# Kernel optimization log

Hardware: AMD Instinct MI355X
Metric: run time of the kernel (lower is better)

The kernel has to match this reference:

```python
import jax, jax.numpy as jnp
import numpy as np


def setup_inputs() -> dict:
    key = jax.random.key(0)
    ks = jax.random.split(key, 6)
    B, T, C, H, E = 4, 2048, 768, 3072, 16
    scale = 0.02
    return {
        "x": jax.random.normal(ks[0], (B, T, C), dtype=jnp.float32),
        "w_shared_fc": jax.random.normal(ks[1], (C, 2 * H), dtype=jnp.float32) * scale,
        "w_shared_proj": jax.random.normal(ks[2], (H, C), dtype=jnp.float32) * scale,
        "w_experts_fc": jax.random.normal(ks[3], (E, C, 2 * H), dtype=jnp.float32) * scale,
        "w_experts_proj": jax.random.normal(ks[4], (E, H, C), dtype=jnp.float32) * scale,
        "w_gate": jax.random.normal(ks[5], (C, E), dtype=jnp.float32) * scale,
        "expert_bias": jnp.zeros((E,), dtype=jnp.float32),
        "top_k": 4,
    }


def _swiglu(h):
    gate, val = jnp.split(h, 2, axis=-1)
    return jax.nn.silu(gate) * val


def reference(x, w_shared_fc, w_shared_proj, w_experts_fc, w_experts_proj,
              w_gate, expert_bias, top_k):
    B, T, C = x.shape
    E = expert_bias.shape[0]
    N = B * T

    # shared expert (applied to every token)
    shared = _swiglu(x @ w_shared_fc) @ w_shared_proj  # [B,T,C]

    # top-k sigmoid routing
    gate_logits = x @ w_gate + expert_bias            # [B,T,E]
    gate_w = jax.nn.sigmoid(gate_logits)
    top_w, top_idx = jax.lax.top_k(gate_w, top_k)     # [B,T,K]
    top_w = top_w / jnp.sum(top_w, axis=-1, keepdims=True)

    # dense per-token/per-expert weight matrix [N,E] (zero for unrouted)
    w_dense = jnp.sum(jax.nn.one_hot(top_idx, E, dtype=x.dtype) * top_w[..., None],
                      axis=-2).reshape(N, E)

    flat_x = x.reshape(N, C)

    def body(acc, params):
        wfc, wproj, we = params  # [C,2H], [H,C], [N]
        out = _swiglu(flat_x @ wfc) @ wproj  # [N,C]
        return acc + we[:, None] * out, None

    routed, _ = jax.lax.scan(body, jnp.zeros_like(flat_x),
                             (w_experts_fc, w_experts_proj, w_dense.T))
    return shared + routed.reshape(B, T, C)
```

## Files before the change

kernel.cpp:

```cpp
#include <hip/hip_runtime.h>
#include <hip/hip_bf16.h>

typedef __hip_bfloat16 bf16;
typedef __attribute__((ext_vector_type(8))) short short8;
typedef __attribute__((ext_vector_type(4))) float float4v;

#define BM 128
#define BK 32

__device__ __forceinline__ void gload16(const bf16* g, bf16* s) {
    __builtin_amdgcn_global_load_lds(
        (const __attribute__((address_space(1))) void*)g,
        (__attribute__((address_space(3))) void*)s, 16, 0, 0);
}


__global__ void k_zero_cnt(int* cnt) {
    if (threadIdx.x < 16) cnt[threadIdx.x] = 0;
}

__global__ void k_convert_x(const float* __restrict__ in, bf16* __restrict__ out, int n) {
    int i = (blockIdx.x * blockDim.x + threadIdx.x) * 4;
    if (i + 3 < n) {
        float4 v = *(const float4*)(in + i);
        out[i + 0] = __float2bfloat16(v.x);
        out[i + 1] = __float2bfloat16(v.y);
        out[i + 2] = __float2bfloat16(v.z);
        out[i + 3] = __float2bfloat16(v.w);
    }
}

__global__ void k_transpose(const float* __restrict__ in, bf16* __restrict__ out,
                            int R, int S) {
    __shared__ float tile[32][33];
    size_t mat = (size_t)blockIdx.z * R * S;
    int s0 = blockIdx.x * 32, r0 = blockIdx.y * 32;
    int tx = threadIdx.x, ty = threadIdx.y;
    #pragma unroll
    for (int i = 0; i < 32; i += 8)
        tile[ty + i][tx] = in[mat + (size_t)(r0 + ty + i) * S + s0 + tx];
    __syncthreads();
    #pragma unroll
    for (int i = 0; i < 32; i += 8)
        out[mat + (size_t)(s0 + ty + i) * R + r0 + tx] = __float2bfloat16(tile[tx][ty + i]);
}

__global__ void k_gate(const float* __restrict__ x, const float* __restrict__ wg,
                       const float* __restrict__ bias, int* __restrict__ cnt,
                       int* __restrict__ tok, float* __restrict__ wl) {
    __shared__ float gates[16][17];
    int t = threadIdx.x;
    int tl = t >> 4;
    int e = t & 15;
    int token = blockIdx.x * 16 + tl;
    const float* xr = x + (size_t)token * 768;
    float acc = 0.f;
    #pragma unroll 4
    for (int c = 0; c < 768; ++c) acc += xr[c] * wg[c * 16 + e];
    acc += bias[e];
    gates[tl][e] = 1.f / (1.f + expf(-acc));
    __syncthreads();
    if (t < 16) {
        int token2 = blockIdx.x * 16 + t;
        float g[16];
        #pragma unroll
        for (int j = 0; j < 16; ++j) g[j] = gates[t][j];
        int idx[4]; float w[4]; float sum = 0.f;
        #pragma unroll
        for (int k = 0; k < 4; ++k) {
            float best = -1e30f; int bi = 0;
            #pragma unroll
            for (int j = 0; j < 16; ++j)
                if (g[j] > best) { best = g[j]; bi = j; }
            idx[k] = bi; w[k] = best; sum += best; g[bi] = -1e30f;
        }
        float inv = 1.f / sum;
        for (int k = 0; k < 4; ++k) {
            int slot = atomicAdd(&cnt[idx[k]], 1);
            tok[(idx[k] << 13) + slot] = token2;
            wl[(idx[k] << 13) + slot] = w[k] * inv;
        }
    }
}

__global__ void k_offsets(const int* __restrict__ cnt, int* __restrict__ offs) {
    if (threadIdx.x == 0) {
        int s = 0;
        for (int e = 0; e < 16; ++e) { offs[e] = s; s += cnt[e]; }
    }
}

template<int GATHER>
__global__ __launch_bounds__(256) void k_fc_swiglu(
    const bf16* __restrict__ A, const bf16* __restrict__ BT,
    bf16* __restrict__ act, const int* __restrict__ cnt,
    const int* __restrict__ offs, const int* __restrict__ tok) {
    const int Kd = 768, H = 3072;
    int e = blockIdx.z;
    int m0 = blockIdx.y * BM;
    int n0 = blockIdx.x * 64;
    int M;
    size_t actbase = 0;
    const int* tl = nullptr;
    if (GATHER) {
        M = cnt[e];
        if (m0 >= M) return;
        tl = tok + (e << 13);
        actbase = (size_t)offs[e] * H;
        BT += (size_t)e * 6144 * Kd;
    } else {
        M = 8192;
    }

    __shared__ bf16 sA[BM * BK];
    __shared__ bf16 sBg[64 * BK];
    __shared__ bf16 sBv[64 * BK];

    int tid = threadIdx.x;
    int lane = tid & 63;
    int w = tid >> 6;
    int wm = w & 1, wn = w >> 1;

    int cA0 = (w << 6) + lane;
    int cA1 = 256 + cA0;
    int cB = (w << 6) + lane;

    int rA0 = cA0 >> 2, rA1 = cA1 >> 2, rB = cB >> 2;
    int kA0 = (cA0 & 3) * 8, kA1 = (cA1 & 3) * 8, kB = (cB & 3) * 8;

    int grA0, grA1;
    if (GATHER) {
        grA0 = tl[min(m0 + rA0, M - 1)];
        grA1 = tl[min(m0 + rA1, M - 1)];
    } else {
        grA0 = m0 + rA0; grA1 = m0 + rA1;
    }

    const bf16* gA0 = A + (size_t)grA0 * Kd + kA0;
    const bf16* gA1 = A + (size_t)grA1 * Kd + kA1;
    const bf16* gBg = BT + (size_t)(n0 + rB) * Kd + kB;
    const bf16* gBv = BT + (size_t)(H + n0 + rB) * Kd + kB;
    bf16* sA0p = sA + cA0 * 8;
    bf16* sA1p = sA + cA1 * 8;
    bf16* sBgp = sBg + cB * 8;
    bf16* sBvp = sBv + cB * 8;

    float4v ag[4][2] = {};
    float4v av[4][2] = {};
    int quad = lane >> 4, l16 = lane & 15;

    for (int k0 = 0; k0 < Kd; k0 += BK) {
        __syncthreads();
        gload16(gA0 + k0, sA0p);
        gload16(gA1 + k0, sA1p);
        gload16(gBg + k0, sBgp);
        gload16(gBv + k0, sBvp);
        __syncthreads();
        short8 af[4], bg[2], bv[2];
        #pragma unroll
        for (int mf = 0; mf < 4; ++mf)
            af[mf] = *(const short8*)(sA + ((wm * 64 + mf * 16 + l16) * BK + quad * 8));
        #pragma unroll
        for (int nf = 0; nf < 2; ++nf) {
            bg[nf] = *(const short8*)(sBg + ((wn * 32 + nf * 16 + l16) * BK + quad * 8));
            bv[nf] = *(const short8*)(sBv + ((wn * 32 + nf * 16 + l16) * BK + quad * 8));
        }
        #pragma unroll
        for (int mf = 0; mf < 4; ++mf)
            #pragma unroll
            for (int nf = 0; nf < 2; ++nf) {
                ag[mf][nf] = __builtin_amdgcn_mfma_f32_16x16x32_bf16(af[mf], bg[nf], ag[mf][nf], 0, 0, 0);
                av[mf][nf] = __builtin_amdgcn_mfma_f32_16x16x32_bf16(af[mf], bv[nf], av[mf][nf], 0, 0, 0);
            }
    }

    #pragma unroll
    for (int mf = 0; mf < 4; ++mf)
        #pragma unroll
        for (int nf = 0; nf < 2; ++nf)
            #pragma unroll
            for (int r = 0; r < 4; ++r) {
                int mrow = m0 + wm * 64 + mf * 16 + quad * 4 + r;
                if (GATHER && mrow >= M) continue;
                int col = n0 + wn * 32 + nf * 16 + l16;
                float g = ag[mf][nf][r];
                float v = av[mf][nf][r];
                float sg = g / (1.f + __expf(-g));
                act[actbase + (size_t)mrow * H + col] = __float2bfloat16(sg * v);
            }
}

template<int ROUTED>
__global__ __launch_bounds__(256) void k_proj(
    const bf16* __restrict__ Aact, const bf16* __restrict__ PT,
    float* __restrict__ out, const int* __restrict__ cnt,
    const int* __restrict__ offs, const int* __restrict__ tok,
    const float* __restrict__ wl) {
    const int Kd = 3072;
    int e = blockIdx.z;
    int m0 = blockIdx.y * BM;
    int n0 = blockIdx.x * BM;
    int M;
    size_t abase = 0;
    if (ROUTED) {
        M = cnt[e];
        if (m0 >= M) return;
        abase = (size_t)offs[e] * Kd;
        PT += (size_t)e * 768 * Kd;
    } else {
        M = 8192;
    }

    __shared__ bf16 sA[BM * BK];
    __shared__ bf16 sB[BM * BK];

    int tid = threadIdx.x, lane = tid & 63, w = tid >> 6;
    int wm = w & 1, wn = w >> 1;
    int c0 = (w << 6) + lane;
    int c1 = 256 + c0;
    int r0 = c0 >> 2, r1 = c1 >> 2;
    int k0c = (c0 & 3) * 8, k1c = (c1 & 3) * 8;

    int ra0 = min(m0 + r0, M - 1);
    int ra1 = min(m0 + r1, M - 1);
    const bf16* gA0 = Aact + abase + (size_t)ra0 * Kd + k0c;
    const bf16* gA1 = Aact + abase + (size_t)ra1 * Kd + k1c;
    const bf16* gB0 = PT + (size_t)(n0 + r0) * Kd + k0c;
    const bf16* gB1 = PT + (size_t)(n0 + r1) * Kd + k1c;
    bf16* sA0p = sA + c0 * 8;
    bf16* sA1p = sA + c1 * 8;
    bf16* sB0p = sB + c0 * 8;
    bf16* sB1p = sB + c1 * 8;

    float4v acc[4][4] = {};
    int quad = lane >> 4, l16 = lane & 15;

    for (int kk = 0; kk < Kd; kk += BK) {
        __syncthreads();
        gload16(gA0 + kk, sA0p);
        gload16(gA1 + kk, sA1p);
        gload16(gB0 + kk, sB0p);
        gload16(gB1 + kk, sB1p);
        __syncthreads();
        short8 af[4], bb[4];
        #pragma unroll
        for (int i = 0; i < 4; ++i) {
            af[i] = *(const short8*)(sA + ((wm * 64 + i * 16 + l16) * BK + quad * 8));
            bb[i] = *(const short8*)(sB + ((wn * 64 + i * 16 + l16) * BK + quad * 8));
        }
        #pragma unroll
        for (int mf = 0; mf < 4; ++mf)
            #pragma unroll
            for (int nf = 0; nf < 4; ++nf)
                acc[mf][nf] = __builtin_amdgcn_mfma_f32_16x16x32_bf16(af[mf], bb[nf], acc[mf][nf], 0, 0, 0);
    }

    #pragma unroll
    for (int mf = 0; mf < 4; ++mf) {
        #pragma unroll
        for (int r = 0; r < 4; ++r) {
            int mr = m0 + wm * 64 + mf * 16 + quad * 4 + r;
            if (ROUTED) {
                if (mr < M) {
                    int t = tok[(e << 13) + mr];
                    float wgt = wl[(e << 13) + mr];
                    #pragma unroll
                    for (int nf = 0; nf < 4; ++nf) {
                        int col = n0 + wn * 64 + nf * 16 + l16;
                        atomicAdd(out + (size_t)t * 768 + col, wgt * acc[mf][nf][r]);
                    }
                }
            } else {
                #pragma unroll
                for (int nf = 0; nf < 4; ++nf) {
                    int col = n0 + wn * 64 + nf * 16 + l16;
                    out[(size_t)mr * 768 + col] = acc[mf][nf][r];
                }
            }
        }
    }
}


extern "C" void kernel_launch(void* const* d_in, const int* in_sizes, int n_in,
                              void* d_out, int out_size, void* d_ws, size_t ws_size,
                              hipStream_t stream) {
    const float* x    = (const float*)d_in[0];
    const float* wfc  = (const float*)d_in[1];
    const float* wpr  = (const float*)d_in[2];
    const float* wefc = (const float*)d_in[3];
    const float* wepr = (const float*)d_in[4];
    const float* wg   = (const float*)d_in[5];
    const float* eb   = (const float*)d_in[6];
    float* out = (float*)d_out;

    char* p = (char*)d_ws;
    bf16* x_bf  = (bf16*)p; p += (size_t)8192 * 768 * 2;
    bf16* fcT_s = (bf16*)p; p += (size_t)6144 * 768 * 2;
    bf16* prT_s = (bf16*)p; p += (size_t)768 * 3072 * 2;
    bf16* fcT_e = (bf16*)p; p += (size_t)16 * 6144 * 768 * 2;
    bf16* prT_e = (bf16*)p; p += (size_t)16 * 768 * 3072 * 2;
    bf16* act_s = (bf16*)p; p += (size_t)8192 * 3072 * 2;
    bf16* act_r = (bf16*)p; p += (size_t)32768 * 3072 * 2;
    int* cnt    = (int*)p;  p += 64;
    int* offs   = (int*)p;  p += 64;
    int* tok    = (int*)p;  p += (size_t)16 * 8192 * 4;
    float* wl   = (float*)p; p += (size_t)16 * 8192 * 4;

    k_zero_cnt<<<dim3(1), dim3(64), 0, stream>>>(cnt);
    k_convert_x<<<dim3(6144), dim3(256), 0, stream>>>(x, x_bf, 8192 * 768);
    k_transpose<<<dim3(192, 24, 1), dim3(32, 8), 0, stream>>>(wfc, fcT_s, 768, 6144);
    k_transpose<<<dim3(24, 96, 1), dim3(32, 8), 0, stream>>>(wpr, prT_s, 3072, 768);
    k_transpose<<<dim3(192, 24, 16), dim3(32, 8), 0, stream>>>(wefc, fcT_e, 768, 6144);
    k_transpose<<<dim3(24, 96, 16), dim3(32, 8), 0, stream>>>(wepr, prT_e, 3072, 768);
    k_gate<<<dim3(512), dim3(256), 0, stream>>>(x, wg, eb, cnt, tok, wl);
    k_offsets<<<dim3(1), dim3(64), 0, stream>>>(cnt, offs);

    k_fc_swiglu<0><<<dim3(48, 64, 1), dim3(256), 0, stream>>>(x_bf, fcT_s, act_s, cnt, offs, tok);
    k_fc_swiglu<1><<<dim3(48, 64, 16), dim3(256), 0, stream>>>(x_bf, fcT_e, act_r, cnt, offs, tok);
    k_proj<0><<<dim3(6, 64, 1), dim3(256), 0, stream>>>(act_s, prT_s, out, cnt, offs, tok, wl);
    k_proj<1><<<dim3(6, 64, 16), dim3(256), 0, stream>>>(act_r, prT_e, out, cnt, offs, tok, wl);
}
```

Baseline: 1.761 ms.

## Enlarge GEMM tiles to 512-thread blocks and swizzle LDS layout

Doubles the FC tile width to 128 columns and the projection tile height to 256 rows, using 8 waves per block so each staged A/B tile is reused by more MFMA work. It also XOR-swizzles the k-chunk placement in shared memory to reduce LDS bank conflicts on the fragment reads. The trade-off is fewer blocks, which means less parallelism for experts with few tokens, along with more LDS and register pressure per block.

New measurement: 1.649 ms. -6.4%, faster.

```diff
diff --git a/kernel.cpp b/kernel.cpp
--- a/kernel.cpp
+++ b/kernel.cpp
@@ -5,7 +5,6 @@
 typedef __attribute__((ext_vector_type(8))) short short8;
 typedef __attribute__((ext_vector_type(4))) float float4v;
 
-#define BM 128
 #define BK 32
 
 __device__ __forceinline__ void gload16(const bf16* g, bf16* s) {
@@ -91,14 +90,14 @@
 }
 
 template<int GATHER>
-__global__ __launch_bounds__(256) void k_fc_swiglu(
+__global__ __launch_bounds__(512) void k_fc_swiglu(
     const bf16* __restrict__ A, const bf16* __restrict__ BT,
     bf16* __restrict__ act, const int* __restrict__ cnt,
     const int* __restrict__ offs, const int* __restrict__ tok) {
     const int Kd = 768, H = 3072;
     int e = blockIdx.z;
-    int m0 = blockIdx.y * BM;
-    int n0 = blockIdx.x * 64;
+    int m0 = blockIdx.y * 128;
+    int n0 = blockIdx.x * 128;
     int M;
     size_t actbase = 0;
     const int* tl = nullptr;
@@ -112,58 +111,48 @@
         M = 8192;
     }
 
-    __shared__ bf16 sA[BM * BK];
-    __shared__ bf16 sBg[64 * BK];
-    __shared__ bf16 sBv[64 * BK];
+    __shared__ bf16 sA[128 * BK];
+    __shared__ bf16 sBg[128 * BK];
+    __shared__ bf16 sBv[128 * BK];
 
     int tid = threadIdx.x;
     int lane = tid & 63;
     int w = tid >> 6;
     int wm = w & 1, wn = w >> 1;
 
-    int cA0 = (w << 6) + lane;
-    int cA1 = 256 + cA0;
-    int cB = (w << 6) + lane;
-
-    int rA0 = cA0 >> 2, rA1 = cA1 >> 2, rB = cB >> 2;
-    int kA0 = (cA0 & 3) * 8, kA1 = (cA1 & 3) * 8, kB = (cB & 3) * 8;
-
-    int grA0, grA1;
-    if (GATHER) {
-        grA0 = tl[min(m0 + rA0, M - 1)];
-        grA1 = tl[min(m0 + rA1, M - 1)];
-    } else {
-        grA0 = m0 + rA0; grA1 = m0 + rA1;
-    }
-
-    const bf16* gA0 = A + (size_t)grA0 * Kd + kA0;
-    const bf16* gA1 = A + (size_t)grA1 * Kd + kA1;
-    const bf16* gBg = BT + (size_t)(n0 + rB) * Kd + kB;
-    const bf16* gBv = BT + (size_t)(H + n0 + rB) * Kd + kB;
-    bf16* sA0p = sA + cA0 * 8;
-    bf16* sA1p = sA + cA1 * 8;
-    bf16* sBgp = sBg + cB * 8;
-    bf16* sBvp = sBv + cB * 8;
+    int sr = tid >> 2;
+    int k2 = (tid & 3) ^ ((sr >> 1) & 3);
+
+    int grA = GATHER ? tl[min(m0 + sr, M - 1)] : (m0 + sr);
+    const bf16* gA  = A  + (size_t)grA * Kd + k2 * 8;
+    const bf16* gBg = BT + (size_t)(n0 + sr) * Kd + k2 * 8;
+    const bf16* gBv = BT + (size_t)(H + n0 + sr) * Kd + k2 * 8;
+    bf16* sAp  = sA  + tid * 8;
+    bf16* sBgp = sBg + tid * 8;
+    bf16* sBvp = sBv + tid * 8;
 
     float4v ag[4][2] = {};
     float4v av[4][2] = {};
     int quad = lane >> 4, l16 = lane & 15;
+    int q2 = quad ^ ((l16 >> 1) & 3);
 
     for (int k0 = 0; k0 < Kd; k0 += BK) {
         __syncthreads();
-        gload16(gA0 + k0, sA0p);
-        gload16(gA1 + k0, sA1p);
+        gload16(gA + k0, sAp);
         gload16(gBg + k0, sBgp);
         gload16(gBv + k0, sBvp);
         __syncthreads();
         short8 af[4], bg[2], bv[2];
         #pragma unroll
-        for (int mf = 0; mf < 4; ++mf)
-            af[mf] = *(const short8*)(sA + ((wm * 64 + mf * 16 + l16) * BK + quad * 8));
+        for (int mf = 0; mf < 4; ++mf) {
+            int row = wm * 64 + mf * 16 + l16;
+            af[mf] = *(const short8*)(sA + row * BK + q2 * 8);
+        }
         #pragma unroll
         for (int nf = 0; nf < 2; ++nf) {
-            bg[nf] = *(const short8*)(sBg + ((wn * 32 + nf * 16 + l16) * BK + quad * 8));
-            bv[nf] = *(const short8*)(sBv + ((wn * 32 + nf * 16 + l16) * BK + quad * 8));
+            int row = wn * 32 + nf * 16 + l16;
+            bg[nf] = *(const short8*)(sBg + row * BK + q2 * 8);
+            bv[nf] = *(const short8*)(sBv + row * BK + q2 * 8);
         }
         #pragma unroll
         for (int mf = 0; mf < 4; ++mf)
@@ -191,15 +180,15 @@
 }
 
 template<int ROUTED>
-__global__ __launch_bounds__(256) void k_proj(
+__global__ __launch_bounds__(512) void k_proj(
     const bf16* __restrict__ Aact, const bf16* __restrict__ PT,
     float* __restrict__ out, const int* __restrict__ cnt,
     const int* __restrict__ offs, const int* __restrict__ tok,
     const float* __restrict__ wl) {
     const int Kd = 3072;
     int e = blockIdx.z;
-    int m0 = blockIdx.y * BM;
-    int n0 = blockIdx.x * BM;
+    int m0 = blockIdx.y * 256;
+    int n0 = blockIdx.x * 128;
     int M;
     size_t abase = 0;
     if (ROUTED) {
@@ -211,42 +200,45 @@
         M = 8192;
     }
 
-    __shared__ bf16 sA[BM * BK];
-    __shared__ bf16 sB[BM * BK];
+    __shared__ bf16 sA[256 * BK];
+    __shared__ bf16 sB[128 * BK];
 
     int tid = threadIdx.x, lane = tid & 63, w = tid >> 6;
-    int wm = w & 1, wn = w >> 1;
-    int c0 = (w << 6) + lane;
-    int c1 = 256 + c0;
-    int r0 = c0 >> 2, r1 = c1 >> 2;
-    int k0c = (c0 & 3) * 8, k1c = (c1 & 3) * 8;
-
-    int ra0 = min(m0 + r0, M - 1);
-    int ra1 = min(m0 + r1, M - 1);
-    const bf16* gA0 = Aact + abase + (size_t)ra0 * Kd + k0c;
-    const bf16* gA1 = Aact + abase + (size_t)ra1 * Kd + k1c;
-    const bf16* gB0 = PT + (size_t)(n0 + r0) * Kd + k0c;
-    const bf16* gB1 = PT + (size_t)(n0 + r1) * Kd + k1c;
-    bf16* sA0p = sA + c0 * 8;
-    bf16* sA1p = sA + c1 * 8;
-    bf16* sB0p = sB + c0 * 8;
-    bf16* sB1p = sB + c1 * 8;
+    int wm = w & 3, wn = w >> 2;
+
+    int srA0 = tid >> 2;
+    int srA1 = (tid + 512) >> 2;
+    int k2A0 = (tid & 3) ^ ((srA0 >> 1) & 3);
+    int k2A1 = (tid & 3) ^ ((srA1 >> 1) & 3);
+    int srB = tid >> 2;
+    int k2B = (tid & 3) ^ ((srB >> 1) & 3);
+
+    int ra0 = min(m0 + srA0, M - 1);
+    int ra1 = min(m0 + srA1, M - 1);
+    const bf16* gA0 = Aact + abase + (size_t)ra0 * Kd + k2A0 * 8;
+    const bf16* gA1 = Aact + abase + (size_t)ra1 * Kd + k2A1 * 8;
+    const bf16* gB  = PT + (size_t)(n0 + srB) * Kd + k2B * 8;
+    bf16* sA0p = sA + tid * 8;
+    bf16* sA1p = sA + (tid + 512) * 8;
+    bf16* sBp  = sB + tid * 8;
 
     float4v acc[4][4] = {};
     int quad = lane >> 4, l16 = lane & 15;
+    int q2 = quad ^ ((l16 >> 1) & 3);
 
     for (int kk = 0; kk < Kd; kk += BK) {
         __syncthreads();
         gload16(gA0 + kk, sA0p);
         gload16(gA1 + kk, sA1p);
-        gload16(gB0 + kk, sB0p);
-        gload16(gB1 + kk, sB1p);
+        gload16(gB + kk, sBp);
         __syncthreads();
         short8 af[4], bb[4];
         #pragma unroll
         for (int i = 0; i < 4; ++i) {
-            af[i] = *(const short8*)(sA + ((wm * 64 + i * 16 + l16) * BK + quad * 8));
-            bb[i] = *(const short8*)(sB + ((wn * 64 + i * 16 + l16) * BK + quad * 8));
+            int rowa = wm * 64 + i * 16 + l16;
+            int rowb = wn * 64 + i * 16 + l16;
+            af[i] = *(const short8*)(sA + rowa * BK + q2 * 8);
+            bb[i] = *(const short8*)(sB + rowb * BK + q2 * 8);
         }
         #pragma unroll
         for (int mf = 0; mf < 4; ++mf)
@@ -316,8 +308,8 @@
     k_gate<<<dim3(512), dim3(256), 0, stream>>>(x, wg, eb, cnt, tok, wl);
     k_offsets<<<dim3(1), dim3(64), 0, stream>>>(cnt, offs);
 
-    k_fc_swiglu<0><<<dim3(48, 64, 1), dim3(256), 0, stream>>>(x_bf, fcT_s, act_s, cnt, offs, tok);
-    k_fc_swiglu<1><<<dim3(48, 64, 16), dim3(256), 0, stream>>>(x_bf, fcT_e, act_r, cnt, offs, tok);
-    k_proj<0><<<dim3(6, 64, 1), dim3(256), 0, stream>>>(act_s, prT_s, out, cnt, offs, tok, wl);
-    k_proj<1><<<dim3(6, 64, 16), dim3(256), 0, stream>>>(act_r, prT_e, out, cnt, offs, tok, wl);
-}
+    k_fc_swiglu<0><<<dim3(24, 64, 1), dim3(512), 0, stream>>>(x_bf, fcT_s, act_s, cnt, offs, tok);
+    k_fc_swiglu<1><<<dim3(24, 64, 16), dim3(512), 0, stream>>>(x_bf, fcT_e, act_r, cnt, offs, tok);
+    k_proj<0><<<dim3(6, 32, 1), dim3(512), 0, stream>>>(act_s, prT_s, out, cnt, offs, tok, wl);
+    k_proj<1><<<dim3(6, 32, 16), dim3(512), 0, stream>>>(act_r, prT_e, out, cnt, offs, tok, wl);
+}
```
